# Kernel tuning notes

Measured on AMD Instinct MI355X. Metric: run time of the kernel, lower is better.

The kernel has to match this reference:

```python
import jax, jax.numpy as jnp
import numpy as np

N_WORDS = 262144
N_TAGS = 512
BDIM = 768
MDIM = 128


def setup_inputs() -> dict:
    key = jax.random.key(0)
    k1, k2, k3, k4, k5, k6 = jax.random.split(key, 6)
    scale = 1.0 / np.sqrt(BDIM)
    return {
        "tags_embed": jax.random.normal(k1, (N_TAGS, BDIM), dtype=jnp.float32),
        "words_embed": jax.random.normal(k2, (N_WORDS, BDIM), dtype=jnp.float32),
        "tags_W": jax.random.normal(k3, (MDIM, BDIM), dtype=jnp.float32) * scale,
        "tags_b": jax.random.normal(k4, (MDIM,), dtype=jnp.float32) * scale,
        "words_W": jax.random.normal(k5, (MDIM, BDIM), dtype=jnp.float32) * scale,
        "words_b": jax.random.normal(k6, (MDIM,), dtype=jnp.float32) * scale,
    }


def reference(tags_embed, words_embed, tags_W, tags_b, words_W, words_b):
    # Linear projections into the metric space: [T, M] and [N, M]
    tags_m = tags_embed @ tags_W.T + tags_b
    words_m = words_embed @ words_W.T + words_b
    # Pairwise squared Euclidean distances via ||w||^2 + ||t||^2 - 2 w.t
    # (same math as the expand-subtract-pow-sum, GEMM-based instead)
    w_sq = jnp.sum(words_m * words_m, axis=1, keepdims=True)  # [N, 1]
    t_sq = jnp.sum(tags_m * tags_m, axis=1)[None, :]          # [1, T]
    distances = w_sq + t_sq - 2.0 * (words_m @ tags_m.T)      # [N, T]
    logits = -distances
    log_pred_y = jax.nn.log_softmax(logits, axis=1)
    pred_y = jax.nn.softmax(logits, axis=1)
    return (log_pred_y, pred_y)
```

## Files before the change

kernel.cpp:

```cpp
#include <hip/hip_runtime.h>

#define N_WORDS 262144
#define N_TAGS  512
#define BDIM    768
#define MDIM    128
#define KS      32
#define NSL     (BDIM / KS)
#define BW      64

typedef __attribute__((ext_vector_type(8))) short  bf16x8;
typedef __attribute__((ext_vector_type(4))) float  f32x4;

#define GLOAD16(ldsdst, gsrc) __builtin_amdgcn_global_load_lds( \
    (const __attribute__((address_space(1))) unsigned int*)(gsrc), \
    (__attribute__((address_space(3))) unsigned int*)(ldsdst), 16, 0, 0)

__device__ inline unsigned bf16_1(float a) {
    union { float f; unsigned u; } ua; ua.f = a;
    unsigned x = ua.u;
    x += 0x7fffu + ((x >> 16) & 1u);
    return x >> 16;
}
__device__ inline unsigned bf16_2(float a, float b) {
    union { float f; unsigned u; } ua, ub; ua.f = a; ub.f = b;
    unsigned x = ua.u, y = ub.u;
    x += 0x7fffu + ((x >> 16) & 1u);
    y += 0x7fffu + ((y >> 16) & 1u);
    return (x >> 16) | (y & 0xffff0000u);
}

__global__ __launch_bounds__(128) void tags_kernel(
    const float* __restrict__ tags_embed, const float* __restrict__ tags_W,
    const float* __restrict__ tags_b, const float* __restrict__ words_b,
    unsigned short* __restrict__ Tbf, float* __restrict__ cvec)
{
    __shared__ __align__(16) float sE[BDIM];
    __shared__ float red[128];
    const int t = blockIdx.x;
    const int m = threadIdx.x;

    for (int i = m; i < BDIM; i += 128) sE[i] = tags_embed[(size_t)t * BDIM + i];
    __syncthreads();

    float acc = tags_b[m];
    const float* Wr = tags_W + (size_t)m * BDIM;
    #pragma unroll 8
    for (int b = 0; b < BDIM; b += 4) {
        float4 w4 = *reinterpret_cast<const float4*>(Wr + b);
        float4 e4 = *reinterpret_cast<const float4*>(&sE[b]);
        acc += w4.x * e4.x + w4.y * e4.y + w4.z * e4.z + w4.w * e4.w;
    }
    Tbf[(size_t)t * MDIM + m] = (unsigned short)bf16_1(2.0f * acc);

    red[m] = acc * (2.0f * words_b[m] - acc);
    __syncthreads();
    for (int s = 64; s > 0; s >>= 1) {
        if (m < s) red[m] += red[m + s];
        __syncthreads();
    }
    if (m == 0) cvec[t] = red[0];
}

__global__ __launch_bounds__(256) void wt_kernel(
    const float* __restrict__ W, unsigned short* __restrict__ Wtbf)
{
    __shared__ float sT[32][33];
    const int bm = blockIdx.x & 3, bk = blockIdx.x >> 2;
    const int m0 = bm * 32, k0 = bk * 32;
    const int r = threadIdx.x >> 3, c = threadIdx.x & 7;

    f32x4 w4 = *reinterpret_cast<const f32x4*>(W + (size_t)(m0 + r) * BDIM + k0 + c * 4);
    sT[r][c * 4 + 0] = w4.x;  sT[r][c * 4 + 1] = w4.y;
    sT[r][c * 4 + 2] = w4.z;  sT[r][c * 4 + 3] = w4.w;
    __syncthreads();

    unsigned lo = bf16_2(sT[c * 4 + 0][r], sT[c * 4 + 1][r]);
    unsigned hi = bf16_2(sT[c * 4 + 2][r], sT[c * 4 + 3][r]);
    unsigned long long p = ((unsigned long long)hi << 32) | lo;
    *reinterpret_cast<unsigned long long*>(Wtbf + (size_t)(k0 + r) * MDIM + m0 + c * 4) = p;
}

__global__ __launch_bounds__(64) void gt_kernel(
    const unsigned short* __restrict__ Wtbf, const unsigned short* __restrict__ Tbf,
    unsigned short* __restrict__ GtSl)
{
    const int kt = blockIdx.x % 48, tg = blockIdx.x / 48;
    const int k0 = kt * 16, t0 = tg * 64;
    const int n = threadIdx.x & 15, q = threadIdx.x >> 4;

    bf16x8 a[4];
    #pragma unroll
    for (int ks = 0; ks < 4; ++ks)
        a[ks] = *reinterpret_cast<const bf16x8*>(
            Wtbf + (size_t)(k0 + n) * MDIM + ks * 32 + q * 8);

    const int s2  = kt >> 1;
    const int off = (kt & 1) * 16 + 4 * q;

    #pragma unroll
    for (int tt = 0; tt < 4; ++tt) {
        f32x4 acc = (f32x4){0.f, 0.f, 0.f, 0.f};
        #pragma unroll
        for (int ks = 0; ks < 4; ++ks) {
            bf16x8 b = *reinterpret_cast<const bf16x8*>(
                Tbf + (size_t)(t0 + tt * 16 + n) * MDIM + ks * 32 + q * 8);
            acc = __builtin_amdgcn_mfma_f32_16x16x32_bf16(a[ks], b, acc, 0, 0, 0);
        }
        unsigned lo = bf16_2(acc.x, acc.y);
        unsigned hi = bf16_2(acc.z, acc.w);
        unsigned long long p = ((unsigned long long)hi << 32) | lo;
        *reinterpret_cast<unsigned long long*>(
            GtSl + (size_t)s2 * (N_TAGS * KS) + (size_t)(t0 + tt * 16 + n) * KS + off) = p;
    }
}

__global__ __launch_bounds__(512, 4) void main_kernel(
    const float* __restrict__ embed,
    const unsigned short* __restrict__ GtSl,
    const float* __restrict__ cvec,
    float* __restrict__ out_logp, float* __restrict__ out_p)
{
    __shared__ __align__(16) unsigned short sG[2 * N_TAGS * KS];
    __shared__ __align__(16) unsigned short sE[2 * BW * KS];
    __shared__ float sMx[8][BW];
    __shared__ float sSm[8][BW];

    const int tid  = threadIdx.x;
    const int lane = tid & 63;
    const int v    = tid >> 6;
    const int n    = lane & 15;
    const int q    = lane >> 4;
    const int we   = tid >> 3;
    const int kp   = tid & 7;
    const int w0   = blockIdx.x * BW;

    const float* eSrc = embed + (size_t)(w0 + we) * BDIM + kp * 4;

    {
        f32x4 e = *reinterpret_cast<const f32x4*>(eSrc);
        unsigned lo = bf16_2(e.x, e.y), hi = bf16_2(e.z, e.w);
        *reinterpret_cast<unsigned long long*>(sE + we * KS + kp * 4) =
            ((unsigned long long)hi << 32) | lo;
        #pragma unroll
        for (int r = 0; r < 4; ++r)
            GLOAD16(sG + (r * 8 + v) * 512,
                    GtSl + (size_t)((r * 8 + v) * 64 + lane) * 8);
    }
    __syncthreads();

    f32x4 acc[4][4];
    #pragma unroll
    for (int mt = 0; mt < 4; ++mt)
        #pragma unroll
        for (int wt = 0; wt < 4; ++wt)
            acc[mt][wt] = (f32x4){0.f, 0.f, 0.f, 0.f};

    int cur = 0;
    for (int s = 0; s < NSL; ++s) {
        const int nxt = cur ^ 1;
        f32x4 e;
        if (s + 1 < NSL) {
            e = *reinterpret_cast<const f32x4*>(eSrc + (s + 1) * KS);
            #pragma unroll
            for (int r = 0; r < 4; ++r)
                GLOAD16(sG + nxt * (N_TAGS * KS) + (r * 8 + v) * 512,
                        GtSl + (size_t)(s + 1) * (N_TAGS * KS)
                             + (size_t)((r * 8 + v) * 64 + lane) * 8);
        }

        const unsigned short* sGc = sG + cur * (N_TAGS * KS);
        const unsigned short* sEc = sE + cur * (BW * KS);
        bf16x8 a[4], b[4];
        #pragma unroll
        for (int mt = 0; mt < 4; ++mt)
            a[mt] = *reinterpret_cast<const bf16x8*>(
                sGc + (v * 64 + mt * 16 + n) * KS + q * 8);
        #pragma unroll
        for (int wt = 0; wt < 4; ++wt)
            b[wt] = *reinterpret_cast<const bf16x8*>(
                sEc + (wt * 16 + n) * KS + q * 8);
        #pragma unroll
        for (int mt = 0; mt < 4; ++mt)
            #pragma unroll
            for (int wt = 0; wt < 4; ++wt)
                acc[mt][wt] = __builtin_amdgcn_mfma_f32_16x16x32_bf16(
                    a[mt], b[wt], acc[mt][wt], 0, 0, 0);

        if (s + 1 < NSL) {
            unsigned lo = bf16_2(e.x, e.y), hi = bf16_2(e.z, e.w);
            *reinterpret_cast<unsigned long long*>(
                sE + nxt * (BW * KS) + we * KS + kp * 4) =
                ((unsigned long long)hi << 32) | lo;
        }
        __syncthreads();
        cur = nxt;
    }

    #pragma unroll
    for (int mt = 0; mt < 4; ++mt) {
        f32x4 c4 = *reinterpret_cast<const f32x4*>(cvec + v * 64 + mt * 16 + 4 * q);
        #pragma unroll
        for (int wt = 0; wt < 4; ++wt) acc[mt][wt] += c4;
    }

    float mx[4], sm[4];
    #pragma unroll
    for (int wt = 0; wt < 4; ++wt) {
        float m = -3.0e38f;
        #pragma unroll
        for (int mt = 0; mt < 4; ++mt)
            m = fmaxf(m, fmaxf(fmaxf(acc[mt][wt].x, acc[mt][wt].y),
                               fmaxf(acc[mt][wt].z, acc[mt][wt].w)));
        m = fmaxf(m, __shfl_xor(m, 16, 64));
        m = fmaxf(m, __shfl_xor(m, 32, 64));
        mx[wt] = m;
        float s = 0.f;
        #pragma unroll
        for (int mt = 0; mt < 4; ++mt)
            s += __expf(acc[mt][wt].x - m) + __expf(acc[mt][wt].y - m)
               + __expf(acc[mt][wt].z - m) + __expf(acc[mt][wt].w - m);
        s += __shfl_xor(s, 16, 64);
        s += __shfl_xor(s, 32, 64);
        sm[wt] = s;
    }
    if (q == 0) {
        #pragma unroll
        for (int wt = 0; wt < 4; ++wt) {
            sMx[v][wt * 16 + n] = mx[wt];
            sSm[v][wt * 16 + n] = sm[wt];
        }
    }
    __syncthreads();

    #pragma unroll
    for (int wt = 0; wt < 4; ++wt) {
        const int wd = wt * 16 + n;
        float M = sMx[0][wd];
        #pragma unroll
        for (int u = 1; u < 8; ++u) M = fmaxf(M, sMx[u][wd]);
        float S = 0.f;
        #pragma unroll
        for (int u = 0; u < 8; ++u) S += sSm[u][wd] * __expf(sMx[u][wd] - M);
        const float neg = M + __logf(S);

        const size_t row = (size_t)(w0 + wd) * N_TAGS + v * 64 + 4 * q;
        #pragma unroll
        for (int mt = 0; mt < 4; ++mt) {
            f32x4 lp, pp;
            lp.x = acc[mt][wt].x - neg;  pp.x = __expf(lp.x);
            lp.y = acc[mt][wt].y - neg;  pp.y = __expf(lp.y);
            lp.z = acc[mt][wt].z - neg;  pp.z = __expf(lp.z);
            lp.w = acc[mt][wt].w - neg;  pp.w = __expf(lp.w);
            *reinterpret_cast<f32x4*>(out_logp + row + mt * 16) = lp;
            *reinterpret_cast<f32x4*>(out_p    + row + mt * 16) = pp;
        }
    }
}

extern "C" void kernel_launch(void* const* d_in, const int* in_sizes, int n_in,
                              void* d_out, int out_size, void* d_ws, size_t ws_size,
                              hipStream_t stream) {
    const float* tags_embed  = (const float*)d_in[0];
    const float* words_embed = (const float*)d_in[1];
    const float* tags_W      = (const float*)d_in[2];
    const float* tags_b      = (const float*)d_in[3];
    const float* words_W     = (const float*)d_in[4];
    const float* words_b     = (const float*)d_in[5];

    float* out_logp = (float*)d_out;
    float* out_p    = out_logp + (size_t)N_WORDS * N_TAGS;

    unsigned short* Tbf  = (unsigned short*)d_ws;
    float*          cvec = (float*)(Tbf + (size_t)N_TAGS * MDIM);
    unsigned short* Wtbf = (unsigned short*)(cvec + N_TAGS);
    unsigned short* GtSl = Wtbf + (size_t)BDIM * MDIM;

    tags_kernel<<<N_TAGS, 128, 0, stream>>>(tags_embed, tags_W, tags_b, words_b, Tbf, cvec);
    wt_kernel<<<96, 256, 0, stream>>>(words_W, Wtbf);
    gt_kernel<<<384, 64, 0, stream>>>(Wtbf, Tbf, GtSl);
    main_kernel<<<N_WORDS / BW, 512, 0, stream>>>(
        words_embed, GtSl, cvec, out_logp, out_p);
}
```

Baseline: 643.7 us.

## Stream tag operand from global into registers and preload word rows per block

Drops the LDS staging of the projected tag matrix: each wave now loads its MFMA A-fragments straight from global/L2 into registers, double-buffered one K-slice ahead. The word block shrinks to 32 rows. All of each thread's embedding row segment is loaded up front, converted to bf16 and held in registers, then written into a padded LDS tile slice by slice. The aim is to cut LDS traffic and footprint and raise occupancy. The cost is more registers, repeated L2 reads of the tag matrix across twice as many blocks, and raw s_barrier asm in place of __syncthreads.

Result: no change. 643.7 us (-0.0%).

```diff
diff --git a/kernel.cpp b/kernel.cpp
--- a/kernel.cpp
+++ b/kernel.cpp
@@ -6,14 +6,11 @@
 #define MDIM    128
 #define KS      32
 #define NSL     (BDIM / KS)
-#define BW      64
+#define BW      32
+#define EPAD    40
 
 typedef __attribute__((ext_vector_type(8))) short  bf16x8;
 typedef __attribute__((ext_vector_type(4))) float  f32x4;
-
-#define GLOAD16(ldsdst, gsrc) __builtin_amdgcn_global_load_lds( \
-    (const __attribute__((address_space(1))) unsigned int*)(gsrc), \
-    (__attribute__((address_space(3))) unsigned int*)(ldsdst), 16, 0, 0)
 
 __device__ inline unsigned bf16_1(float a) {
     union { float f; unsigned u; } ua; ua.f = a;
@@ -120,8 +117,7 @@
     const float* __restrict__ cvec,
     float* __restrict__ out_logp, float* __restrict__ out_p)
 {
-    __shared__ __align__(16) unsigned short sG[2 * N_TAGS * KS];
-    __shared__ __align__(16) unsigned short sE[2 * BW * KS];
+    __shared__ __align__(16) unsigned short sE[2][BW * EPAD];
     __shared__ float sMx[8][BW];
     __shared__ float sSm[8][BW];
 
@@ -130,82 +126,85 @@
     const int v    = tid >> 6;
     const int n    = lane & 15;
     const int q    = lane >> 4;
-    const int we   = tid >> 3;
-    const int kp   = tid & 7;
+    const int we   = tid >> 4;
+    const int kp   = tid & 15;
     const int w0   = blockIdx.x * BW;
 
-    const float* eSrc = embed + (size_t)(w0 + we) * BDIM + kp * 4;
-
+    unsigned pk[24];
     {
-        f32x4 e = *reinterpret_cast<const f32x4*>(eSrc);
-        unsigned lo = bf16_2(e.x, e.y), hi = bf16_2(e.z, e.w);
-        *reinterpret_cast<unsigned long long*>(sE + we * KS + kp * 4) =
-            ((unsigned long long)hi << 32) | lo;
-        #pragma unroll
-        for (int r = 0; r < 4; ++r)
-            GLOAD16(sG + (r * 8 + v) * 512,
-                    GtSl + (size_t)((r * 8 + v) * 64 + lane) * 8);
-    }
-    __syncthreads();
-
-    f32x4 acc[4][4];
+        const float* eS = embed + (size_t)(w0 + we) * BDIM + kp * 4;
+        f32x4 e[12];
+        #pragma unroll
+        for (int r = 0; r < 12; ++r)
+            e[r] = *reinterpret_cast<const f32x4*>(eS + r * 64);
+        #pragma unroll
+        for (int r = 0; r < 12; ++r) {
+            pk[2 * r]     = bf16_2(e[r].x, e[r].y);
+            pk[2 * r + 1] = bf16_2(e[r].z, e[r].w);
+        }
+    }
+
+    if (kp < 8)
+        *reinterpret_cast<unsigned long long*>(&sE[0][we * EPAD + (kp & 7) * 4]) =
+            ((unsigned long long)pk[1] << 32) | pk[0];
+
+    const unsigned short* Ab = GtSl + (size_t)(v * 64 + n) * KS + q * 8;
+    bf16x8 aC[4], aN[4];
     #pragma unroll
     for (int mt = 0; mt < 4; ++mt)
-        #pragma unroll
-        for (int wt = 0; wt < 4; ++wt)
-            acc[mt][wt] = (f32x4){0.f, 0.f, 0.f, 0.f};
-
-    int cur = 0;
+        aC[mt] = *reinterpret_cast<const bf16x8*>(Ab + mt * 512);
+
+    asm volatile("s_waitcnt lgkmcnt(0)\n\ts_barrier" ::: "memory");
+
+    f32x4 acc[4][2];
+    #pragma unroll
+    for (int mt = 0; mt < 4; ++mt) {
+        acc[mt][0] = (f32x4){0.f, 0.f, 0.f, 0.f};
+        acc[mt][1] = (f32x4){0.f, 0.f, 0.f, 0.f};
+    }
+
+    #pragma unroll
     for (int s = 0; s < NSL; ++s) {
-        const int nxt = cur ^ 1;
-        f32x4 e;
+        const int cur = s & 1;
+
         if (s + 1 < NSL) {
-            e = *reinterpret_cast<const f32x4*>(eSrc + (s + 1) * KS);
+            if ((kp >> 3) == ((s + 1) & 1)) {
+                const int r = (s + 1) >> 1;
+                *reinterpret_cast<unsigned long long*>(
+                    &sE[cur ^ 1][we * EPAD + (kp & 7) * 4]) =
+                    ((unsigned long long)pk[2 * r + 1] << 32) | pk[2 * r];
+            }
             #pragma unroll
-            for (int r = 0; r < 4; ++r)
-                GLOAD16(sG + nxt * (N_TAGS * KS) + (r * 8 + v) * 512,
-                        GtSl + (size_t)(s + 1) * (N_TAGS * KS)
-                             + (size_t)((r * 8 + v) * 64 + lane) * 8);
-        }
-
-        const unsigned short* sGc = sG + cur * (N_TAGS * KS);
-        const unsigned short* sEc = sE + cur * (BW * KS);
-        bf16x8 a[4], b[4];
-        #pragma unroll
-        for (int mt = 0; mt < 4; ++mt)
-            a[mt] = *reinterpret_cast<const bf16x8*>(
-                sGc + (v * 64 + mt * 16 + n) * KS + q * 8);
-        #pragma unroll
-        for (int wt = 0; wt < 4; ++wt)
-            b[wt] = *reinterpret_cast<const bf16x8*>(
-                sEc + (wt * 16 + n) * KS + q * 8);
-        #pragma unroll
-        for (int mt = 0; mt < 4; ++mt)
+            for (int mt = 0; mt < 4; ++mt)
+                aN[mt] = *reinterpret_cast<const bf16x8*>(
+                    Ab + (size_t)(s + 1) * (N_TAGS * KS) + mt * 512);
+        }
+
+        bf16x8 b0 = *reinterpret_cast<const bf16x8*>(&sE[cur][n * EPAD + q * 8]);
+        bf16x8 b1 = *reinterpret_cast<const bf16x8*>(&sE[cur][(16 + n) * EPAD + q * 8]);
+        #pragma unroll
+        for (int mt = 0; mt < 4; ++mt) {
+            acc[mt][0] = __builtin_amdgcn_mfma_f32_16x16x32_bf16(aC[mt], b0, acc[mt][0], 0, 0, 0);
+            acc[mt][1] = __builtin_amdgcn_mfma_f32_16x16x32_bf16(aC[mt], b1, acc[mt][1], 0, 0, 0);
+        }
+
+        if (s + 1 < NSL) {
+            asm volatile("s_waitcnt lgkmcnt(0)\n\ts_barrier" ::: "memory");
             #pragma unroll
-            for (int wt = 0; wt < 4; ++wt)
-                acc[mt][wt] = __builtin_amdgcn_mfma_f32_16x16x32_bf16(
-                    a[mt], b[wt], acc[mt][wt], 0, 0, 0);
-
-        if (s + 1 < NSL) {
-            unsigned lo = bf16_2(e.x, e.y), hi = bf16_2(e.z, e.w);
-            *reinterpret_cast<unsigned long long*>(
-                sE + nxt * (BW * KS) + we * KS + kp * 4) =
-                ((unsigned long long)hi << 32) | lo;
-        }
-        __syncthreads();
-        cur = nxt;
+            for (int mt = 0; mt < 4; ++mt) aC[mt] = aN[mt];
+        }
     }
 
     #pragma unroll
     for (int mt = 0; mt < 4; ++mt) {
         f32x4 c4 = *reinterpret_cast<const f32x4*>(cvec + v * 64 + mt * 16 + 4 * q);
-        #pragma unroll
-        for (int wt = 0; wt < 4; ++wt) acc[mt][wt] += c4;
-    }
-
-    float mx[4], sm[4];
-    #pragma unroll
-    for (int wt = 0; wt < 4; ++wt) {
+        acc[mt][0] += c4;
+        acc[mt][1] += c4;
+    }
+
+    float mx[2], sm[2];
+    #pragma unroll
+    for (int wt = 0; wt < 2; ++wt) {
         float m = -3.0e38f;
         #pragma unroll
         for (int mt = 0; mt < 4; ++mt)
@@ -224,16 +223,15 @@
         sm[wt] = s;
     }
     if (q == 0) {
-        #pragma unroll
-        for (int wt = 0; wt < 4; ++wt) {
-            sMx[v][wt * 16 + n] = mx[wt];
-            sSm[v][wt * 16 + n] = sm[wt];
-        }
-    }
-    __syncthreads();
-
-    #pragma unroll
-    for (int wt = 0; wt < 4; ++wt) {
+        sMx[v][n]      = mx[0];
+        sMx[v][16 + n] = mx[1];
+        sSm[v][n]      = sm[0];
+        sSm[v][16 + n] = sm[1];
+    }
+    __syncthreads();
+
+    #pragma unroll
+    for (int wt = 0; wt < 2; ++wt) {
         const int wd = wt * 16 + n;
         float M = sMx[0][wd];
         #pragma unroll
```

## Load tag operand directly to registers, swizzle LDS embed tile, deepen prefetch

Applied to the files above, without the earlier changes.

Removes the LDS staging of the tag-projection slice (sG), so each wave loads its own bf16 A fragments straight from global/L2 into registers one slice ahead. The embedding tile in LDS gets an XOR swizzle to cut bank conflicts, and embedding loads are prefetched three slices ahead. The generic __syncthreads is replaced by a raw s_waitcnt lgkmcnt(0) + s_barrier, and the slice loop is fully unrolled. This frees a large amount of LDS, which could allow more occupancy, and removes LDS round-trips. In exchange it adds register pressure and relies on L2 to serve the A fragments that every block re-reads. The raw barrier does not wait on vmcnt, which is safe only because the global loads land in registers.

Result: faster. 615.9 us (-4.3%).

```diff
diff --git a/kernel.cpp b/kernel.cpp
--- a/kernel.cpp
+++ b/kernel.cpp
@@ -11,10 +11,6 @@
 typedef __attribute__((ext_vector_type(8))) short  bf16x8;
 typedef __attribute__((ext_vector_type(4))) float  f32x4;
 
-#define GLOAD16(ldsdst, gsrc) __builtin_amdgcn_global_load_lds( \
-    (const __attribute__((address_space(1))) unsigned int*)(gsrc), \
-    (__attribute__((address_space(3))) unsigned int*)(ldsdst), 16, 0, 0)
-
 __device__ inline unsigned bf16_1(float a) {
     union { float f; unsigned u; } ua; ua.f = a;
     unsigned x = ua.u;
@@ -120,8 +116,7 @@
     const float* __restrict__ cvec,
     float* __restrict__ out_logp, float* __restrict__ out_p)
 {
-    __shared__ __align__(16) unsigned short sG[2 * N_TAGS * KS];
-    __shared__ __align__(16) unsigned short sE[2 * BW * KS];
+    __shared__ __align__(16) unsigned short sE[2][BW * KS];
     __shared__ float sMx[8][BW];
     __shared__ float sSm[8][BW];
 
@@ -135,18 +130,23 @@
     const int w0   = blockIdx.x * BW;
 
     const float* eSrc = embed + (size_t)(w0 + we) * BDIM + kp * 4;
-
+    const int wrOff = we * KS + (((kp * 8) ^ ((we & 3) << 4)) >> 1);
+
+    const unsigned short* Ab = GtSl + (size_t)(v * 64 + n) * KS + q * 8;
+
+    f32x4 e0 = *reinterpret_cast<const f32x4*>(eSrc);
+    bf16x8 aC[4], aN[4];
+    #pragma unroll
+    for (int mt = 0; mt < 4; ++mt)
+        aC[mt] = *reinterpret_cast<const bf16x8*>(Ab + mt * (16 * KS));
+    f32x4 eA = *reinterpret_cast<const f32x4*>(eSrc + KS);
+    f32x4 eB = *reinterpret_cast<const f32x4*>(eSrc + 2 * KS);
     {
-        f32x4 e = *reinterpret_cast<const f32x4*>(eSrc);
-        unsigned lo = bf16_2(e.x, e.y), hi = bf16_2(e.z, e.w);
-        *reinterpret_cast<unsigned long long*>(sE + we * KS + kp * 4) =
+        unsigned lo = bf16_2(e0.x, e0.y), hi = bf16_2(e0.z, e0.w);
+        *reinterpret_cast<unsigned long long*>(&sE[0][wrOff]) =
             ((unsigned long long)hi << 32) | lo;
-        #pragma unroll
-        for (int r = 0; r < 4; ++r)
-            GLOAD16(sG + (r * 8 + v) * 512,
-                    GtSl + (size_t)((r * 8 + v) * 64 + lane) * 8);
-    }
-    __syncthreads();
+    }
+    asm volatile("s_waitcnt lgkmcnt(0)\n\ts_barrier" ::: "memory");
 
     f32x4 acc[4][4];
     #pragma unroll
@@ -155,45 +155,45 @@
         for (int wt = 0; wt < 4; ++wt)
             acc[mt][wt] = (f32x4){0.f, 0.f, 0.f, 0.f};
 
-    int cur = 0;
+    #pragma unroll
     for (int s = 0; s < NSL; ++s) {
-        const int nxt = cur ^ 1;
-        f32x4 e;
+        const int cur = s & 1;
+
+        f32x4 eN;
+        if (s + 3 < NSL)
+            eN = *reinterpret_cast<const f32x4*>(eSrc + (s + 3) * KS);
+
         if (s + 1 < NSL) {
-            e = *reinterpret_cast<const f32x4*>(eSrc + (s + 1) * KS);
             #pragma unroll
-            for (int r = 0; r < 4; ++r)
-                GLOAD16(sG + nxt * (N_TAGS * KS) + (r * 8 + v) * 512,
-                        GtSl + (size_t)(s + 1) * (N_TAGS * KS)
-                             + (size_t)((r * 8 + v) * 64 + lane) * 8);
-        }
-
-        const unsigned short* sGc = sG + cur * (N_TAGS * KS);
-        const unsigned short* sEc = sE + cur * (BW * KS);
-        bf16x8 a[4], b[4];
-        #pragma unroll
-        for (int mt = 0; mt < 4; ++mt)
-            a[mt] = *reinterpret_cast<const bf16x8*>(
-                sGc + (v * 64 + mt * 16 + n) * KS + q * 8);
-        #pragma unroll
-        for (int wt = 0; wt < 4; ++wt)
+            for (int mt = 0; mt < 4; ++mt)
+                aN[mt] = *reinterpret_cast<const bf16x8*>(
+                    Ab + (size_t)(s + 1) * (N_TAGS * KS) + mt * (16 * KS));
+            unsigned lo = bf16_2(eA.x, eA.y), hi = bf16_2(eA.z, eA.w);
+            *reinterpret_cast<unsigned long long*>(&sE[cur ^ 1][wrOff]) =
+                ((unsigned long long)hi << 32) | lo;
+        }
+
+        bf16x8 b[4];
+        #pragma unroll
+        for (int wt = 0; wt < 4; ++wt) {
+            const int R = wt * 16 + n;
             b[wt] = *reinterpret_cast<const bf16x8*>(
-                sEc + (wt * 16 + n) * KS + q * 8);
+                &sE[cur][R * KS + (((q * 16) ^ ((R & 3) << 4)) >> 1)]);
+        }
         #pragma unroll
         for (int mt = 0; mt < 4; ++mt)
             #pragma unroll
             for (int wt = 0; wt < 4; ++wt)
                 acc[mt][wt] = __builtin_amdgcn_mfma_f32_16x16x32_bf16(
-                    a[mt], b[wt], acc[mt][wt], 0, 0, 0);
+                    aC[mt], b[wt], acc[mt][wt], 0, 0, 0);
 
         if (s + 1 < NSL) {
-            unsigned lo = bf16_2(e.x, e.y), hi = bf16_2(e.z, e.w);
-            *reinterpret_cast<unsigned long long*>(
-                sE + nxt * (BW * KS) + we * KS + kp * 4) =
-                ((unsigned long long)hi << 32) | lo;
-        }
-        __syncthreads();
-        cur = nxt;
+            asm volatile("s_waitcnt lgkmcnt(0)\n\ts_barrier" ::: "memory");
+            eA = eB;
+            #pragma unroll
+            for (int mt = 0; mt < 4; ++mt) aC[mt] = aN[mt];
+        }
+        if (s + 3 < NSL) eB = eN;
     }
 
     #pragma unroll
```

## Use 1024-thread blocks with a triple-buffered G pipeline and manual waitcnt barriers

Applied to the files above, without the earlier changes.

The main kernel now runs 1024 threads per block, so each wave handles 32 tags instead of 64. The precomputed G slices are triple-buffered in LDS with a two-slice prefetch distance, and hand-written s_waitcnt vmcnt(3)+s_barrier replaces __syncthreads so the loads in flight stay outstanding. The embedding is loaded with nontemporal float2 loads. The aim is to hide global latency and raise the number of waves in flight, at the cost of more LDS per block (about 104KB), which may limit occupancy to one block per CU, plus a 16-way cross-wave softmax reduction.

New measurement: 677.5 us. 5.2% more time.

```diff
diff --git a/kernel.cpp b/kernel.cpp
--- a/kernel.cpp
+++ b/kernel.cpp
@@ -7,9 +7,11 @@
 #define KS      32
 #define NSL     (BDIM / KS)
 #define BW      64
+#define SLB     (N_TAGS * KS)
 
 typedef __attribute__((ext_vector_type(8))) short  bf16x8;
 typedef __attribute__((ext_vector_type(4))) float  f32x4;
+typedef __attribute__((ext_vector_type(2))) float  f32x2;
 
 #define GLOAD16(ldsdst, gsrc) __builtin_amdgcn_global_load_lds( \
     (const __attribute__((address_space(1))) unsigned int*)(gsrc), \
@@ -27,6 +29,9 @@
     x += 0x7fffu + ((x >> 16) & 1u);
     y += 0x7fffu + ((y >> 16) & 1u);
     return (x >> 16) | (y & 0xffff0000u);
+}
+__device__ inline f32x2 ntld2(const float* p) {
+    return __builtin_nontemporal_load(reinterpret_cast<const f32x2*>(p));
 }
 
 __global__ __launch_bounds__(128) void tags_kernel(
@@ -110,124 +115,134 @@
         unsigned hi = bf16_2(acc.z, acc.w);
         unsigned long long p = ((unsigned long long)hi << 32) | lo;
         *reinterpret_cast<unsigned long long*>(
-            GtSl + (size_t)s2 * (N_TAGS * KS) + (size_t)(t0 + tt * 16 + n) * KS + off) = p;
-    }
-}
-
-__global__ __launch_bounds__(512, 4) void main_kernel(
+            GtSl + (size_t)s2 * SLB + (size_t)(t0 + tt * 16 + n) * KS + off) = p;
+    }
+}
+
+__global__ __launch_bounds__(1024, 4) void main_kernel(
     const float* __restrict__ embed,
     const unsigned short* __restrict__ GtSl,
     const float* __restrict__ cvec,
     float* __restrict__ out_logp, float* __restrict__ out_p)
 {
-    __shared__ __align__(16) unsigned short sG[2 * N_TAGS * KS];
+    __shared__ __align__(16) unsigned short sG[3 * SLB];
     __shared__ __align__(16) unsigned short sE[2 * BW * KS];
-    __shared__ float sMx[8][BW];
-    __shared__ float sSm[8][BW];
+    __shared__ float sMx[16 * 64];
+    __shared__ float sSm[16 * 64];
 
     const int tid  = threadIdx.x;
     const int lane = tid & 63;
     const int v    = tid >> 6;
     const int n    = lane & 15;
     const int q    = lane >> 4;
-    const int we   = tid >> 3;
-    const int kp   = tid & 7;
+    const int we   = tid >> 4;
+    const int kp   = tid & 15;
     const int w0   = blockIdx.x * BW;
 
-    const float* eSrc = embed + (size_t)(w0 + we) * BDIM + kp * 4;
+    const float* eSrc = embed + (size_t)(w0 + we) * BDIM + kp * 2;
 
     {
-        f32x4 e = *reinterpret_cast<const f32x4*>(eSrc);
-        unsigned lo = bf16_2(e.x, e.y), hi = bf16_2(e.z, e.w);
-        *reinterpret_cast<unsigned long long*>(sE + we * KS + kp * 4) =
-            ((unsigned long long)hi << 32) | lo;
-        #pragma unroll
-        for (int r = 0; r < 4; ++r)
-            GLOAD16(sG + (r * 8 + v) * 512,
-                    GtSl + (size_t)((r * 8 + v) * 64 + lane) * 8);
-    }
-    __syncthreads();
-
-    f32x4 acc[4][4];
-    #pragma unroll
-    for (int mt = 0; mt < 4; ++mt)
+        f32x2 e0 = ntld2(eSrc);
+        #pragma unroll
+        for (int r = 0; r < 2; ++r)
+            GLOAD16(sG + (r * 16 + v) * 512,
+                    GtSl + (size_t)((r * 16 + v) * 64 + lane) * 8);
+        #pragma unroll
+        for (int r = 0; r < 2; ++r)
+            GLOAD16(sG + SLB + (r * 16 + v) * 512,
+                    GtSl + (size_t)SLB + (size_t)((r * 16 + v) * 64 + lane) * 8);
+        *reinterpret_cast<unsigned*>(sE + we * KS + kp * 2) = bf16_2(e0.x, e0.y);
+        asm volatile("s_waitcnt vmcnt(0) lgkmcnt(0)\n\ts_barrier" ::: "memory");
+    }
+    f32x2 eOld = ntld2(eSrc + KS);
+
+    f32x4 acc[2][4];
+    #pragma unroll
+    for (int mt = 0; mt < 2; ++mt)
         #pragma unroll
         for (int wt = 0; wt < 4; ++wt)
             acc[mt][wt] = (f32x4){0.f, 0.f, 0.f, 0.f};
 
-    int cur = 0;
-    for (int s = 0; s < NSL; ++s) {
-        const int nxt = cur ^ 1;
-        f32x4 e;
-        if (s + 1 < NSL) {
-            e = *reinterpret_cast<const f32x4*>(eSrc + (s + 1) * KS);
-            #pragma unroll
-            for (int r = 0; r < 4; ++r)
-                GLOAD16(sG + nxt * (N_TAGS * KS) + (r * 8 + v) * 512,
-                        GtSl + (size_t)(s + 1) * (N_TAGS * KS)
-                             + (size_t)((r * 8 + v) * 64 + lane) * 8);
-        }
-
-        const unsigned short* sGc = sG + cur * (N_TAGS * KS);
-        const unsigned short* sEc = sE + cur * (BW * KS);
-        bf16x8 a[4], b[4];
-        #pragma unroll
-        for (int mt = 0; mt < 4; ++mt)
-            a[mt] = *reinterpret_cast<const bf16x8*>(
-                sGc + (v * 64 + mt * 16 + n) * KS + q * 8);
-        #pragma unroll
-        for (int wt = 0; wt < 4; ++wt)
-            b[wt] = *reinterpret_cast<const bf16x8*>(
-                sEc + (wt * 16 + n) * KS + q * 8);
-        #pragma unroll
-        for (int mt = 0; mt < 4; ++mt)
-            #pragma unroll
-            for (int wt = 0; wt < 4; ++wt)
-                acc[mt][wt] = __builtin_amdgcn_mfma_f32_16x16x32_bf16(
-                    a[mt], b[wt], acc[mt][wt], 0, 0, 0);
-
-        if (s + 1 < NSL) {
-            unsigned lo = bf16_2(e.x, e.y), hi = bf16_2(e.z, e.w);
-            *reinterpret_cast<unsigned long long*>(
-                sE + nxt * (BW * KS) + we * KS + kp * 4) =
-                ((unsigned long long)hi << 32) | lo;
-        }
-        __syncthreads();
-        cur = nxt;
-    }
-
-    #pragma unroll
-    for (int mt = 0; mt < 4; ++mt) {
-        f32x4 c4 = *reinterpret_cast<const f32x4*>(cvec + v * 64 + mt * 16 + 4 * q);
+    int esel = 0;
+
+#define SLICE(SV, RB, DB, ISSUE, VMC)                                        \
+    {                                                                        \
+        f32x2 eN;                                                            \
+        if (ISSUE) {                                                         \
+            eN = ntld2(eSrc + ((SV) + 2) * KS);                              \
+            _Pragma("unroll")                                                \
+            for (int r = 0; r < 2; ++r)                                      \
+                GLOAD16(sG + (DB) * SLB + (r * 16 + v) * 512,                \
+                        GtSl + (size_t)((SV) + 2) * SLB                      \
+                             + (size_t)((r * 16 + v) * 64 + lane) * 8);      \
+        }                                                                    \
+        if ((SV) + 1 < NSL)                                                  \
+            *reinterpret_cast<unsigned*>(                                    \
+                sE + (esel ^ 1) * (BW * KS) + we * KS + kp * 2) =            \
+                bf16_2(eOld.x, eOld.y);                                      \
+        {                                                                    \
+            const unsigned short* sGc = sG + (RB) * SLB;                     \
+            const unsigned short* sEc = sE + esel * (BW * KS);               \
+            bf16x8 a0 = *reinterpret_cast<const bf16x8*>(                    \
+                sGc + (v * 32 + n) * KS + q * 8);                            \
+            bf16x8 a1 = *reinterpret_cast<const bf16x8*>(                    \
+                sGc + (v * 32 + 16 + n) * KS + q * 8);                       \
+            _Pragma("unroll")                                                \
+            for (int wt = 0; wt < 4; ++wt) {                                 \
+                bf16x8 b = *reinterpret_cast<const bf16x8*>(                 \
+                    sEc + (wt * 16 + n) * KS + q * 8);                       \
+                acc[0][wt] = __builtin_amdgcn_mfma_f32_16x16x32_bf16(        \
+                    a0, b, acc[0][wt], 0, 0, 0);                             \
+                acc[1][wt] = __builtin_amdgcn_mfma_f32_16x16x32_bf16(        \
+                    a1, b, acc[1][wt], 0, 0, 0);                             \
+            }                                                                \
+        }                                                                    \
+        if ((VMC) == 3)                                                      \
+            asm volatile("s_waitcnt vmcnt(3) lgkmcnt(0)\n\ts_barrier" ::: "memory"); \
+        else if ((VMC) == 0)                                                 \
+            asm volatile("s_waitcnt vmcnt(0) lgkmcnt(0)\n\ts_barrier" ::: "memory"); \
+        if (ISSUE) eOld = eN;                                                \
+        esel ^= 1;                                                           \
+    }
+
+    #pragma unroll 1
+    for (int j = 0; j < 7; ++j) {
+        const int s0 = 3 * j;
+        SLICE(s0,     0, 2, 1, 3)
+        SLICE(s0 + 1, 1, 0, 1, 3)
+        SLICE(s0 + 2, 2, 1, 1, 3)
+    }
+    SLICE(21, 0, 2, 1, 3)
+    SLICE(22, 1, 2, 0, 0)
+    SLICE(23, 2, 2, 0, -1)
+#undef SLICE
+
+    #pragma unroll
+    for (int mt = 0; mt < 2; ++mt) {
+        f32x4 c4 = *reinterpret_cast<const f32x4*>(cvec + v * 32 + mt * 16 + 4 * q);
         #pragma unroll
         for (int wt = 0; wt < 4; ++wt) acc[mt][wt] += c4;
     }
 
-    float mx[4], sm[4];
     #pragma unroll
     for (int wt = 0; wt < 4; ++wt) {
         float m = -3.0e38f;
         #pragma unroll
-        for (int mt = 0; mt < 4; ++mt)
+        for (int mt = 0; mt < 2; ++mt)
             m = fmaxf(m, fmaxf(fmaxf(acc[mt][wt].x, acc[mt][wt].y),
                                fmaxf(acc[mt][wt].z, acc[mt][wt].w)));
         m = fmaxf(m, __shfl_xor(m, 16, 64));
         m = fmaxf(m, __shfl_xor(m, 32, 64));
-        mx[wt] = m;
-        float s = 0.f;
-        #pragma unroll
-        for (int mt = 0; mt < 4; ++mt)
-            s += __expf(acc[mt][wt].x - m) + __expf(acc[mt][wt].y - m)
-               + __expf(acc[mt][wt].z - m) + __expf(acc[mt][wt].w - m);
-        s += __shfl_xor(s, 16, 64);
-        s += __shfl_xor(s, 32, 64);
-        sm[wt] = s;
-    }
-    if (q == 0) {
-        #pragma unroll
-        for (int wt = 0; wt < 4; ++wt) {
-            sMx[v][wt * 16 + n] = mx[wt];
-            sSm[v][wt * 16 + n] = sm[wt];
+        float ss = 0.f;
+        #pragma unroll
+        for (int mt = 0; mt < 2; ++mt)
+            ss += __expf(acc[mt][wt].x - m) + __expf(acc[mt][wt].y - m)
+                + __expf(acc[mt][wt].z - m) + __expf(acc[mt][wt].w - m);
+        ss += __shfl_xor(ss, 16, 64);
+        ss += __shfl_xor(ss, 32, 64);
+        if (q == 0) {
+            sMx[v * 64 + wt * 16 + n] = m;
+            sSm[v * 64 + wt * 16 + n] = ss;
         }
     }
     __syncthreads();
@@ -235,24 +250,24 @@
     #pragma unroll
     for (int wt = 0; wt < 4; ++wt) {
         const int wd = wt * 16 + n;
-        float M = sMx[0][wd];
-        #pragma unroll
-        for (int u = 1; u < 8; ++u) M = fmaxf(M, sMx[u][wd]);
+        float M = sMx[wd];
+        #pragma unroll
+        for (int u = 1; u < 16; ++u) M = fmaxf(M, sMx[u * 64 + wd]);
         float S = 0.f;
         #pragma unroll
-        for (int u = 0; u < 8; ++u) S += sSm[u][wd] * __expf(sMx[u][wd] - M);
+        for (int u = 0; u < 16; ++u)
+            S += sSm[u * 64 + wd] * __expf(sMx[u * 64 + wd] - M);
         const float neg = M + __logf(S);
 
-        const size_t row = (size_t)(w0 + wd) * N_TAGS + v * 64 + 4 * q;
-        #pragma unroll
-        for (int mt = 0; mt < 4; ++mt) {
-            f32x4 lp, pp;
-            lp.x = acc[mt][wt].x - neg;  pp.x = __expf(lp.x);
-            lp.y = acc[mt][wt].y - neg;  pp.y = __expf(lp.y);
-            lp.z = acc[mt][wt].z - neg;  pp.z = __expf(lp.z);
-            lp.w = acc[mt][wt].w - neg;  pp.w = __expf(lp.w);
-            *reinterpret_cast<f32x4*>(out_logp + row + mt * 16) = lp;
-            *reinterpret_cast<f32x4*>(out_p    + row + mt * 16) = pp;
+        const size_t rb = (size_t)(w0 + wd) * N_TAGS + v * 32 + 4 * q;
+        #pragma unroll
+        for (int mt = 0; mt < 2; ++mt) {
+            f32x4 d = acc[mt][wt] - neg;
+            *reinterpret_cast<f32x4*>(out_logp + rb + mt * 16) = d;
+            f32x4 e;
+            e.x = __expf(d.x); e.y = __expf(d.y);
+            e.z = __expf(d.z); e.w = __expf(d.w);
+            *reinterpret_cast<f32x4*>(out_p + rb + mt * 16) = e;
         }
     }
 }
@@ -278,6 +293,6 @@
     tags_kernel<<<N_TAGS, 128, 0, stream>>>(tags_embed, tags_W, tags_b, words_b, Tbf, cvec);
     wt_kernel<<<96, 256, 0, stream>>>(words_W, Wtbf);
     gt_kernel<<<384, 64, 0, stream>>>(Wtbf, Tbf, GtSl);
-    main_kernel<<<N_WORDS / BW, 512, 0, stream>>>(
+    main_kernel<<<N_WORDS / BW, 1024, 0, stream>>>(
         words_embed, GtSl, cvec, out_logp, out_p);
 }
```
